# Kernel optimization log

Measured on AMD Instinct MI355X. Metric: run time of the kernel, lower is better.

## Reference

```python
import jax, jax.numpy as jnp
import numpy as np

B, HI, WI, DIM = 4, 128, 128, 128
HO, WO = HI // 2, WI // 2
NUM_ITERS = 3
EPS_LN, EPS_A = 1e-5, 1e-6


def _nbr_idx(H, W):
    # NATTEN kernel_size=3 neighborhood with border clamping: window center is
    # clip(i, 1, H-2) so every position sees exactly 9 neighbors.
    r = 1
    ci = jnp.clip(jnp.arange(H), r, H - 1 - r)
    cj = jnp.clip(jnp.arange(W), r, W - 1 - r)
    off = jnp.arange(-1, 2)
    ri = ci[:, None] + off[None, :]  # (H,3)
    rj = cj[:, None] + off[None, :]  # (W,3)
    nbr = jnp.broadcast_to(ri[:, None, :, None], (H, W, 3, 3)).reshape(H, W, 9)
    nbc = jnp.broadcast_to(rj[None, :, None, :], (H, W, 3, 3)).reshape(H, W, 9)
    return nbr, nbc


def _ln(x, g, b):
    mu = jnp.mean(x, -1, keepdims=True)
    var = jnp.mean(jnp.square(x - mu), -1, keepdims=True)
    return (x - mu) * jax.lax.rsqrt(var + EPS_LN) * g + b


def setup_inputs() -> dict:
    key = jax.random.key(0)
    ks = jax.random.split(key, 10)
    s = DIM ** -0.5
    return {
        "x": jax.random.normal(ks[0], (B, HI * WI, DIM), jnp.float32),
        "conv_w": jax.random.normal(ks[1], (DIM, DIM, 3, 3), jnp.float32) * (2.0 / (DIM * 9)) ** 0.5,
        "q_w": jax.random.normal(ks[2], (DIM, DIM), jnp.float32) * s,
        "k_w": jax.random.normal(ks[3], (DIM, DIM), jnp.float32) * s,
        "v_w": jax.random.normal(ks[4], (DIM, DIM), jnp.float32) * s,
        "mlp_w1": jax.random.normal(ks[5], (DIM, 2 * DIM), jnp.float32) * s,
        "mlp_b1": jnp.zeros((2 * DIM,), jnp.float32),
        "mlp_w2": jax.random.normal(ks[6], (2 * DIM, DIM), jnp.float32) * (2 * DIM) ** -0.5,
        "mlp_b2": jnp.zeros((DIM,), jnp.float32),
        "ln_in_g": jnp.ones((DIM,), jnp.float32),
        "ln_in_b": jnp.zeros((DIM,), jnp.float32),
        "ln_out_g": jnp.ones((DIM,), jnp.float32),
        "ln_out_b": jnp.zeros((DIM,), jnp.float32),
        "tau": jnp.asarray(np.log(DIM ** -0.5), jnp.float32),
        "rpb": jax.random.normal(ks[7], (4, 9), jnp.float32) * 0.02,
    }


def reference(x, conv_w, q_w, k_w, v_w, mlp_w1, mlp_b1, mlp_w2, mlp_b2,
              ln_in_g, ln_in_b, ln_out_g, ln_out_b, tau, rpb):
    Bx = x.shape[0]
    nbr, nbc = _nbr_idx(HO, WO)
    q_idx = (nbr * WO + nbc).reshape(HO * WO, 9)  # flat seed index of each neighbor

    def to_groups(t):  # (B, Hi*Wi, D) -> (B, 4, Ho, Wo, D); 4 = 2x2 patch pixels (row-major)
        m = t.transpose(0, 2, 1).reshape(Bx, DIM, HO, 2, WO, 2)
        return m.transpose(0, 3, 5, 2, 4, 1).reshape(Bx, 4, HO, WO, DIM)

    k = to_groups(_ln(x, ln_in_g, ln_in_b) @ k_w)
    v = to_groups(x @ v_w)
    v_nb = v[:, :, nbr, nbc, :]  # (B,4,Ho,Wo,9,D) value neighborhoods (loop-invariant)

    x_map = x.transpose(0, 2, 1).reshape(Bx, DIM, HI, WI)
    seed = jax.lax.conv_general_dilated(x_map, conv_w, (2, 2), ((1, 1), (1, 1)),
                                        dimension_numbers=('NCHW', 'OIHW', 'NCHW'))
    x_out = _ln(seed.reshape(Bx, DIM, HO * WO).transpose(0, 2, 1), ln_out_g, ln_out_b)

    scale = jnp.exp(tau)
    flat_idx = jnp.broadcast_to(q_idx[None], (4, HO * WO, 9)).reshape(-1)
    attn = A_col = None
    for _ in range(NUM_ITERS):
        q = _ln(x_out, ln_out_g, ln_out_b) @ q_w
        q_nb = q.reshape(Bx, HO, WO, DIM)[:, nbr, nbc, :]  # (B,Ho,Wo,9,D)
        # na2d_qk(query=k, key=q): logits at key-grid position vs seed neighbors
        attn = jnp.einsum('bghwd,bhwtd->bghwt', k, q_nb)
        attn = jax.nn.softmax((attn + rpb.reshape(1, 4, 1, 1, 9)) * scale, axis=-1) + EPS_A
        # scatter-based column sums over seed tokens (doubly-stochastic step)
        attn_flat = attn.reshape(Bx, -1)
        col_sums = jax.vmap(
            lambda a: jax.ops.segment_sum(a, flat_idx, num_segments=HO * WO))(attn_flat)
        denom = col_sums[:, q_idx]  # (B, Ho*Wo, 9) gather back per-edge
        A_col = (attn.reshape(Bx, 4, HO * WO, 9) / (denom[:, None] + 1e-8)).reshape(Bx, 4, HO, WO, 9)
        # na2d_av(A_col, v) then sum over the 4 patch-pixel groups
        upd = jnp.einsum('bghwt,bghwtd->bhwd', A_col, v_nb).reshape(Bx, HO * WO, DIM)
        x_out = x_out + upd
        h = jax.nn.gelu(x_out @ mlp_w1 + mlp_b1, approximate=False) @ mlp_w2 + mlp_b2
        x_out = x_out + _ln(h, ln_out_g, ln_out_b)
    return x_out, attn, A_col
```

## Files before the change

### kernel.cpp

```cpp
#include <hip/hip_runtime.h>
#include <hip/hip_bf16.h>
#include <math.h>

#define BN 4
#define HIq 128
#define WIq 128
#define DIM 128
#define HOq 64
#define WOq 64
#define NPOS 4096
#define NTOK 16384
#define EPS_LN 1e-5f
#define EPS_A 1e-6f

typedef __attribute__((ext_vector_type(8))) short bf16x8;
typedef __attribute__((ext_vector_type(4))) float f32x4;

__device__ __forceinline__ unsigned short f2bf(float f) {
    unsigned int u = __float_as_uint(f);
    u = (u + 0x7FFFu + ((u >> 16) & 1u)) >> 16;
    return (unsigned short)u;
}

__device__ __forceinline__ float bf2f(unsigned short u) {
    return __uint_as_float((unsigned int)u << 16);
}

__device__ __forceinline__ int nb_index(int h, int w, int t) {
    int ch = min(max(h, 1), HOq - 2);
    int cw = min(max(w, 1), WOq - 2);
    int dr = t / 3 - 1, dc = t % 3 - 1;
    return (ch + dr) * WOq + (cw + dc);
}

__global__ void prep_ln_kernel(const float* __restrict__ x,
                               const float* __restrict__ g,
                               const float* __restrict__ bb,
                               unsigned short* __restrict__ x_bf,
                               unsigned short* __restrict__ xln_bf) {
    int tid = threadIdx.x, wv = tid >> 6, lane = tid & 63;
    long row = (long)blockIdx.x * 4 + wv;
    const float2* xr = (const float2*)(x + row * DIM);
    float2 v = xr[lane];
    float s = v.x + v.y, ss = v.x * v.x + v.y * v.y;
    #pragma unroll
    for (int off = 32; off; off >>= 1) {
        s  += __shfl_xor(s, off, 64);
        ss += __shfl_xor(ss, off, 64);
    }
    float mu = s * (1.0f / DIM);
    float var = fmaxf(ss * (1.0f / DIM) - mu * mu, 0.0f);
    float rstd = rsqrtf(var + EPS_LN);
    float2 gg = ((const float2*)g)[lane];
    float2 bv = ((const float2*)bb)[lane];
    unsigned int xo = (unsigned int)f2bf(v.x) | ((unsigned int)f2bf(v.y) << 16);
    *(unsigned int*)&x_bf[row * DIM + 2 * lane] = xo;
    unsigned int lo = (unsigned int)f2bf((v.x - mu) * rstd * gg.x + bv.x)
                    | ((unsigned int)f2bf((v.y - mu) * rstd * gg.y + bv.y) << 16);
    *(unsigned int*)&xln_bf[row * DIM + 2 * lane] = lo;
}

__global__ void wt_prep_kernel(const float* __restrict__ cw,
                               const float* __restrict__ kw, const float* __restrict__ vw,
                               const float* __restrict__ qw,
                               const float* __restrict__ w1, const float* __restrict__ w2,
                               unsigned short* __restrict__ wt,
                               unsigned short* __restrict__ kwt, unsigned short* __restrict__ vwt,
                               unsigned short* __restrict__ qwt,
                               unsigned short* __restrict__ w1t, unsigned short* __restrict__ w2t) {
    int o = blockIdx.x, i = threadIdx.x;
    #pragma unroll
    for (int tap = 0; tap < 9; ++tap)
        wt[(long)o * 1152 + tap * 128 + i] = f2bf(cw[((long)o * 128 + i) * 9 + tap]);
    kwt[o * DIM + i] = f2bf(kw[i * DIM + o]);
    vwt[o * DIM + i] = f2bf(vw[i * DIM + o]);
    qwt[o * DIM + i] = f2bf(qw[i * DIM + o]);
    w1t[(2 * o) * DIM + i]     = f2bf(w1[i * 256 + 2 * o]);
    w1t[(2 * o + 1) * DIM + i] = f2bf(w1[i * 256 + 2 * o + 1]);
    w2t[o * 256 + i]       = f2bf(w2[i * DIM + o]);
    w2t[o * 256 + 128 + i] = f2bf(w2[(128 + i) * DIM + o]);
}

__global__ __launch_bounds__(256) void conv_mfma_kernel(
        const unsigned short* __restrict__ x_bf,
        const unsigned short* __restrict__ wt,
        const float* __restrict__ ln_g, const float* __restrict__ ln_b,
        float* __restrict__ out_x) {
    __shared__ __align__(16) char smem[52224];
    unsigned short (*As)[136] = (unsigned short(*)[136])smem;
    unsigned short (*Bs)[136] = (unsigned short(*)[136])(smem + 17408);
    float (*o_s)[132]         = (float(*)[132])smem;

    int tid = threadIdx.x;
    int wv = tid >> 6, lane = tid & 63;
    int quad = lane >> 4, l15 = lane & 15;
    int wr = wv >> 1, wc = wv & 1;
    int b = blockIdx.x >> 6, ho = blockIdx.x & 63;

    f32x4 acc[2][4];
    #pragma unroll
    for (int mt = 0; mt < 2; ++mt)
        #pragma unroll
        for (int nt = 0; nt < 4; ++nt) acc[mt][nt] = (f32x4){0.f, 0.f, 0.f, 0.f};

    for (int tap = 0; tap < 9; ++tap) {
        int kh = tap / 3, kw = tap % 3;
        int hi = 2 * ho - 1 + kh;
        bool hok = (hi >= 0) && (hi < HIq);
        __syncthreads();
        #pragma unroll
        for (int it = 0; it < 4; ++it) {
            int c = it * 256 + tid;
            int row = c >> 4, sg = c & 15;
            int wi = 2 * row - 1 + kw;
            int4 av = {0, 0, 0, 0};
            if (hok && wi >= 0 && wi < WIq)
                av = *(const int4*)(x_bf + (((long)b * HIq + hi) * WIq + wi) * DIM + sg * 8);
            *(int4*)&As[row][sg * 8] = av;
        }
        #pragma unroll
        for (int it = 0; it < 8; ++it) {
            int c = it * 256 + tid;
            int row = c >> 4, sg = c & 15;
            *(int4*)&Bs[row][sg * 8] =
                *(const int4*)(wt + (long)row * 1152 + tap * 128 + sg * 8);
        }
        __syncthreads();
        #pragma unroll
        for (int ib = 0; ib < 4; ++ib) {
            bf16x8 afr[2], bfr[4];
            #pragma unroll
            for (int mt = 0; mt < 2; ++mt)
                afr[mt] = *(bf16x8*)&As[wr * 32 + mt * 16 + l15][ib * 32 + quad * 8];
            #pragma unroll
            for (int nt = 0; nt < 4; ++nt)
                bfr[nt] = *(bf16x8*)&Bs[wc * 64 + nt * 16 + l15][ib * 32 + quad * 8];
            #pragma unroll
            for (int mt = 0; mt < 2; ++mt)
                #pragma unroll
                for (int nt = 0; nt < 4; ++nt)
                    acc[mt][nt] = __builtin_amdgcn_mfma_f32_16x16x32_bf16(
                        afr[mt], bfr[nt], acc[mt][nt], 0, 0, 0);
        }
    }
    __syncthreads();
    #pragma unroll
    for (int mt = 0; mt < 2; ++mt)
        #pragma unroll
        for (int r = 0; r < 4; ++r) {
            int wo = wr * 32 + mt * 16 + quad * 4 + r;
            #pragma unroll
            for (int nt = 0; nt < 4; ++nt) {
                int col = wc * 64 + nt * 16 + l15;
                o_s[wo][col] = acc[mt][nt][r];
            }
        }
    __syncthreads();

    {
        int r = tid >> 2, qq = tid & 3;
        float s = 0.f, ss = 0.f;
        #pragma unroll
        for (int j = 0; j < 32; ++j) {
            float v = o_s[r][qq * 32 + j];
            s += v; ss += v * v;
        }
        s  += __shfl_xor(s, 1, 64);  ss += __shfl_xor(ss, 1, 64);
        s  += __shfl_xor(s, 2, 64);  ss += __shfl_xor(ss, 2, 64);
        float mu = s * (1.0f / DIM);
        float var = fmaxf(ss * (1.0f / DIM) - mu * mu, 0.0f);
        float rstd = rsqrtf(var + EPS_LN);
        long outb = ((long)b * NPOS + ho * WOq) * DIM;
        float* xr = out_x + outb + (long)r * DIM + qq * 32;
        #pragma unroll
        for (int j = 0; j < 32; ++j) {
            int c = qq * 32 + j;
            xr[j] = (o_s[r][c] - mu) * rstd * ln_g[c] + ln_b[c];
        }
    }
}

__global__ __launch_bounds__(256) void kv_mfma_kernel(
        const unsigned short* __restrict__ x_bf,
        const unsigned short* __restrict__ xln_bf,
        const unsigned short* __restrict__ kwt,
        const unsigned short* __restrict__ vwt,
        unsigned short* __restrict__ k_bf, unsigned short* __restrict__ v_bf) {
    __shared__ unsigned short Ak[64][40], Av[64][40];
    __shared__ unsigned short Bk[128][40], Bv[128][40];
    int tid = threadIdx.x;
    int wv = tid >> 6, lane = tid & 63;
    int quad = lane >> 4, l15 = lane & 15;
    int wr = wv >> 1, wc = wv & 1;
    long tokBase = (long)blockIdx.x * 64;

    f32x4 acck[2][4], accv[2][4];
    #pragma unroll
    for (int mt = 0; mt < 2; ++mt)
        #pragma unroll
        for (int nt = 0; nt < 4; ++nt) {
            acck[mt][nt] = (f32x4){0.f, 0.f, 0.f, 0.f};
            accv[mt][nt] = (f32x4){0.f, 0.f, 0.f, 0.f};
        }

    int m = tid >> 2, seg = tid & 3;
    #pragma unroll
    for (int ib = 0; ib < 4; ++ib) {
        __syncthreads();
        *(int4*)&Ak[m][seg * 8] = *(const int4*)(xln_bf + (tokBase + m) * DIM + ib * 32 + seg * 8);
        *(int4*)&Av[m][seg * 8] = *(const int4*)(x_bf   + (tokBase + m) * DIM + ib * 32 + seg * 8);
        #pragma unroll
        for (int r2 = 0; r2 < 2; ++r2) {
            int lin = r2 * 256 + tid;
            int n = lin >> 2, sg = lin & 3;
            *(int4*)&Bk[n][sg * 8] = *(const int4*)(kwt + (long)n * DIM + ib * 32 + sg * 8);
            *(int4*)&Bv[n][sg * 8] = *(const int4*)(vwt + (long)n * DIM + ib * 32 + sg * 8);
        }
        __syncthreads();
        bf16x8 ak[2], av2[2], bk[4], bv[4];
        #pragma unroll
        for (int mt = 0; mt < 2; ++mt) {
            ak[mt]  = *(bf16x8*)&Ak[wr * 32 + mt * 16 + l15][quad * 8];
            av2[mt] = *(bf16x8*)&Av[wr * 32 + mt * 16 + l15][quad * 8];
        }
        #pragma unroll
        for (int nt = 0; nt < 4; ++nt) {
            bk[nt] = *(bf16x8*)&Bk[wc * 64 + nt * 16 + l15][quad * 8];
            bv[nt] = *(bf16x8*)&Bv[wc * 64 + nt * 16 + l15][quad * 8];
        }
        #pragma unroll
        for (int mt = 0; mt < 2; ++mt)
            #pragma unroll
            for (int nt = 0; nt < 4; ++nt) {
                acck[mt][nt] = __builtin_amdgcn_mfma_f32_16x16x32_bf16(ak[mt],  bk[nt], acck[mt][nt], 0, 0, 0);
                accv[mt][nt] = __builtin_amdgcn_mfma_f32_16x16x32_bf16(av2[mt], bv[nt], accv[mt][nt], 0, 0, 0);
            }
    }
    #pragma unroll
    for (int mt = 0; mt < 2; ++mt)
        #pragma unroll
        for (int r = 0; r < 4; ++r) {
            long tok = tokBase + wr * 32 + mt * 16 + quad * 4 + r;
            int b = (int)(tok >> 14);
            int pix = (int)(tok & 16383);
            int ih = pix >> 7, iw = pix & 127;
            int g = (ih & 1) * 2 + (iw & 1);
            int pos = (ih >> 1) * WOq + (iw >> 1);
            long base = ((long)(b * 4 + g) * NPOS + pos) * DIM;
            #pragma unroll
            for (int nt = 0; nt < 4; ++nt) {
                int col = wc * 64 + nt * 16 + l15;
                k_bf[base + col] = f2bf(acck[mt][nt][r]);
                v_bf[base + col] = f2bf(accv[mt][nt][r]);
            }
        }
}

__global__ __launch_bounds__(256) void q_mfma_kernel(
        const float* __restrict__ x_out,
        const unsigned short* __restrict__ qwt,
        const float* __restrict__ ln_g, const float* __restrict__ ln_b,
        unsigned short* __restrict__ q,
        float* __restrict__ col_sums) {
    __shared__ unsigned short sxbf[64][136];
    int tid = threadIdx.x;
    long base = (long)blockIdx.x * 64;

    int zi = blockIdx.x * 256 + tid;
    if (zi < BN * NPOS) col_sums[zi] = 0.0f;

    {
        int r = tid >> 2, qq = tid & 3;
        const float* xr = x_out + (base + r) * DIM + qq * 32;
        float vv[32];
        float s = 0.f, ss = 0.f;
        #pragma unroll
        for (int j = 0; j < 8; ++j) {
            float4 v4 = *(const float4*)(xr + j * 4);
            vv[j * 4 + 0] = v4.x; vv[j * 4 + 1] = v4.y;
            vv[j * 4 + 2] = v4.z; vv[j * 4 + 3] = v4.w;
            s += v4.x + v4.y + v4.z + v4.w;
            ss += v4.x * v4.x + v4.y * v4.y + v4.z * v4.z + v4.w * v4.w;
        }
        s  += __shfl_xor(s, 1, 64);  ss += __shfl_xor(ss, 1, 64);
        s  += __shfl_xor(s, 2, 64);  ss += __shfl_xor(ss, 2, 64);
        float mu = s * (1.0f / DIM);
        float var = fmaxf(ss * (1.0f / DIM) - mu * mu, 0.0f);
        float rstd = rsqrtf(var + EPS_LN);
        #pragma unroll
        for (int j = 0; j < 32; ++j) {
            int c = qq * 32 + j;
            sxbf[r][c] = f2bf((vv[j] - mu) * rstd * ln_g[c] + ln_b[c]);
        }
    }
    __syncthreads();

    int wv = tid >> 6, lane = tid & 63;
    int quad = lane >> 4, l15 = lane & 15;
    f32x4 acc[4][2];
    #pragma unroll
    for (int mt = 0; mt < 4; ++mt)
        #pragma unroll
        for (int nt = 0; nt < 2; ++nt) acc[mt][nt] = (f32x4){0.f, 0.f, 0.f, 0.f};

    #pragma unroll
    for (int kb = 0; kb < 4; ++kb) {
        bf16x8 afr[4], bfr[2];
        #pragma unroll
        for (int mt = 0; mt < 4; ++mt)
            afr[mt] = *(bf16x8*)&sxbf[mt * 16 + l15][kb * 32 + quad * 8];
        #pragma unroll
        for (int nt = 0; nt < 2; ++nt) {
            int n = wv * 32 + nt * 16 + l15;
            bfr[nt] = *(const bf16x8*)(qwt + (long)n * DIM + kb * 32 + quad * 8);
        }
        #pragma unroll
        for (int mt = 0; mt < 4; ++mt)
            #pragma unroll
            for (int nt = 0; nt < 2; ++nt)
                acc[mt][nt] = __builtin_amdgcn_mfma_f32_16x16x32_bf16(
                    afr[mt], bfr[nt], acc[mt][nt], 0, 0, 0);
    }
    #pragma unroll
    for (int mt = 0; mt < 4; ++mt)
        #pragma unroll
        for (int r = 0; r < 4; ++r) {
            long tok = base + mt * 16 + quad * 4 + r;
            #pragma unroll
            for (int nt = 0; nt < 2; ++nt) {
                int col = wv * 32 + nt * 16 + l15;
                q[tok * DIM + col] = f2bf(acc[mt][nt][r]);
            }
        }
}

__global__ __launch_bounds__(256) void attn_mfma_kernel(
        const unsigned short* __restrict__ k_bf,
        const unsigned short* __restrict__ q_bf,
        const float* __restrict__ rpb,
        const float* __restrict__ tau,
        float* __restrict__ attn_out,
        float* __restrict__ col_sums) {
    __shared__ __align__(16) char smem[69632];
    __shared__ float colacc[192];
    unsigned short (*Ks)[136] = (unsigned short(*)[136])smem;
    unsigned short (*Qs)[136] = (unsigned short(*)[136])(smem + 17408);
    float (*S)[193]           = (float(*)[193])smem;

    int tid = threadIdx.x;
    int bid = blockIdx.x;
    int h = bid & 63, g = (bid >> 6) & 3, b = bid >> 8;
    int r0 = min(max(h, 1), HOq - 2) - 1;

    long kbase = ((long)(b * 4 + g) * NPOS + h * 64) * DIM;
    long qbase = ((long)b * NPOS + r0 * 64) * DIM;

    if (tid < 192) colacc[tid] = 0.f;

    #pragma unroll
    for (int it = 0; it < 4; ++it) {
        int lin = it * 256 + tid;
        int row = lin >> 4, sg = lin & 15;
        *(int4*)&Ks[row][sg * 8] = *(const int4*)(k_bf + kbase + (long)row * DIM + sg * 8);
    }
    #pragma unroll
    for (int it = 0; it < 12; ++it) {
        int lin = it * 256 + tid;
        int row = lin >> 4, sg = lin & 15;
        *(int4*)&Qs[row][sg * 8] = *(const int4*)(q_bf + qbase + (long)row * DIM + sg * 8);
    }
    __syncthreads();

    int wv = tid >> 6, lane = tid & 63;
    int quad = lane >> 4, l15 = lane & 15;
    f32x4 acc[4][3];
    #pragma unroll
    for (int mt = 0; mt < 4; ++mt)
        #pragma unroll
        for (int nt = 0; nt < 3; ++nt) acc[mt][nt] = (f32x4){0.f, 0.f, 0.f, 0.f};

    #pragma unroll
    for (int kb = 0; kb < 4; ++kb) {
        bf16x8 afr[4], bfr[3];
        #pragma unroll
        for (int mt = 0; mt < 4; ++mt)
            afr[mt] = *(bf16x8*)&Ks[mt * 16 + l15][kb * 32 + quad * 8];
        #pragma unroll
        for (int nt = 0; nt < 3; ++nt)
            bfr[nt] = *(bf16x8*)&Qs[wv * 48 + nt * 16 + l15][kb * 32 + quad * 8];
        #pragma unroll
        for (int mt = 0; mt < 4; ++mt)
            #pragma unroll
            for (int nt = 0; nt < 3; ++nt)
                acc[mt][nt] = __builtin_amdgcn_mfma_f32_16x16x32_bf16(
                    afr[mt], bfr[nt], acc[mt][nt], 0, 0, 0);
    }
    __syncthreads();
    #pragma unroll
    for (int mt = 0; mt < 4; ++mt)
        #pragma unroll
        for (int nt = 0; nt < 3; ++nt)
            #pragma unroll
            for (int r = 0; r < 4; ++r)
                S[mt * 16 + quad * 4 + r][wv * 48 + nt * 16 + l15] = acc[mt][nt][r];
    __syncthreads();

    if (tid < 64) {
        int w = tid;
        int cw = min(max(w, 1), WOq - 2);
        float scale = expf(tau[0]);
        float l[9];
        #pragma unroll
        for (int t = 0; t < 9; ++t) {
            int j = (t / 3) * 64 + cw - 1 + (t % 3);
            l[t] = (S[w][j] + rpb[g * 9 + t]) * scale;
        }
        float m = l[0];
        #pragma unroll
        for (int t = 1; t < 9; ++t) m = fmaxf(m, l[t]);
        float e[9], s = 0.f;
        #pragma unroll
        for (int t = 0; t < 9; ++t) { e[t] = __expf(l[t] - m); s += e[t]; }
        float inv = 1.0f / s;
        long cell = (long)(b * 4 + g) * NPOS + h * 64 + w;
        #pragma unroll
        for (int t = 0; t < 9; ++t) {
            float a = e[t] * inv + EPS_A;
            int j = (t / 3) * 64 + cw - 1 + (t % 3);
            attn_out[cell * 9 + t] = a;
            atomicAdd(&colacc[j], a);
        }
    }
    __syncthreads();
    if (tid < 192) atomicAdd(&col_sums[b * NPOS + r0 * 64 + tid], colacc[tid]);
}

__global__ void acol_upd_kernel(const float* __restrict__ attn_out,
                                const float* __restrict__ col_sums,
                                const unsigned short* __restrict__ v_bf,
                                float* __restrict__ acol_out,
                                float* __restrict__ x_out) {
    __shared__ float sA[36];
    int tid = threadIdx.x;
    int row = blockIdx.x;
    int b = row >> 12, pos = row & 4095;
    int h = pos >> 6, w = pos & 63;

    if (tid < 36) {
        int g = tid / 9, t = tid % 9;
        long ci = ((long)(b * 4 + g) * NPOS + pos) * 9 + t;
        float a = attn_out[ci];
        float cs = col_sums[b * NPOS + nb_index(h, w, t)];
        float A = a / (cs + 1e-8f);
        sA[tid] = A;
        acol_out[ci] = A;
    }
    __syncthreads();

    int nn[9];
    #pragma unroll
    for (int t = 0; t < 9; ++t) nn[t] = nb_index(h, w, t);

    float acc = 0.f;
    #pragma unroll
    for (int g = 0; g < 4; ++g) {
        const unsigned short* vb = v_bf + (long)(b * 4 + g) * NPOS * DIM;
        #pragma unroll
        for (int t = 0; t < 9; ++t) {
            acc += sA[g * 9 + t] * bf2f(vb[(long)nn[t] * DIM + tid]);
        }
    }
    x_out[(long)row * DIM + tid] += acc;
}

__global__ __launch_bounds__(256) void mlp_mfma_kernel(
        float* __restrict__ x_out,
        const unsigned short* __restrict__ w1t,
        const unsigned short* __restrict__ w2t,
        const float* __restrict__ b1, const float* __restrict__ b2,
        const float* __restrict__ ln_g, const float* __restrict__ ln_b) {
    __shared__ __align__(16) char smem[25600];
    unsigned short (*sxbf)[136] = (unsigned short(*)[136])smem;
    unsigned short (*h_s)[264]  = (unsigned short(*)[264])(smem + 8704);
    float (*o_s)[132]           = (float(*)[132])smem;

    int tid = threadIdx.x;
    long base = (long)blockIdx.x * 32;
    int wv = tid >> 6, lane = tid & 63;
    int quad = lane >> 4, l15 = lane & 15;

    {
        int r = tid >> 3, seg = tid & 7;
        const float* xr = x_out + (base + r) * DIM + seg * 16;
        #pragma unroll
        for (int j = 0; j < 2; ++j) {
            float4 a = *(const float4*)(xr + j * 8);
            float4 c = *(const float4*)(xr + j * 8 + 4);
            unsigned short u[8] = {f2bf(a.x), f2bf(a.y), f2bf(a.z), f2bf(a.w),
                                   f2bf(c.x), f2bf(c.y), f2bf(c.z), f2bf(c.w)};
            *(int4*)&sxbf[r][seg * 16 + j * 8] = *(int4*)u;
        }
    }
    __syncthreads();

    f32x4 acc1[2][4];
    #pragma unroll
    for (int mt = 0; mt < 2; ++mt)
        #pragma unroll
        for (int nt = 0; nt < 4; ++nt) acc1[mt][nt] = (f32x4){0.f, 0.f, 0.f, 0.f};
    #pragma unroll
    for (int kb = 0; kb < 4; ++kb) {
        bf16x8 afr[2], bfr[4];
        #pragma unroll
        for (int mt = 0; mt < 2; ++mt)
            afr[mt] = *(bf16x8*)&sxbf[mt * 16 + l15][kb * 32 + quad * 8];
        #pragma unroll
        for (int nt = 0; nt < 4; ++nt) {
            int n = wv * 64 + nt * 16 + l15;
            bfr[nt] = *(const bf16x8*)(w1t + (long)n * DIM + kb * 32 + quad * 8);
        }
        #pragma unroll
        for (int mt = 0; mt < 2; ++mt)
            #pragma unroll
            for (int nt = 0; nt < 4; ++nt)
                acc1[mt][nt] = __builtin_amdgcn_mfma_f32_16x16x32_bf16(
                    afr[mt], bfr[nt], acc1[mt][nt], 0, 0, 0);
    }
    #pragma unroll
    for (int nt = 0; nt < 4; ++nt) {
        int col = wv * 64 + nt * 16 + l15;
        float bj = b1[col];
        #pragma unroll
        for (int mt = 0; mt < 2; ++mt)
            #pragma unroll
            for (int r = 0; r < 4; ++r) {
                int row = mt * 16 + quad * 4 + r;
                float hv = acc1[mt][nt][r] + bj;
                hv = 0.5f * hv * (1.0f + erff(hv * 0.70710678118654752f));
                h_s[row][col] = f2bf(hv);
            }
    }
    __syncthreads();

    f32x4 acc2[2][2];
    #pragma unroll
    for (int mt = 0; mt < 2; ++mt)
        #pragma unroll
        for (int nt = 0; nt < 2; ++nt) acc2[mt][nt] = (f32x4){0.f, 0.f, 0.f, 0.f};
    #pragma unroll
    for (int kb = 0; kb < 8; ++kb) {
        bf16x8 afr[2], bfr[2];
        #pragma unroll
        for (int mt = 0; mt < 2; ++mt)
            afr[mt] = *(bf16x8*)&h_s[mt * 16 + l15][kb * 32 + quad * 8];
        #pragma unroll
        for (int nt = 0; nt < 2; ++nt) {
            int n = wv * 32 + nt * 16 + l15;
            bfr[nt] = *(const bf16x8*)(w2t + (long)n * 256 + kb * 32 + quad * 8);
        }
        #pragma unroll
        for (int mt = 0; mt < 2; ++mt)
            #pragma unroll
            for (int nt = 0; nt < 2; ++nt)
                acc2[mt][nt] = __builtin_amdgcn_mfma_f32_16x16x32_bf16(
                    afr[mt], bfr[nt], acc2[mt][nt], 0, 0, 0);
    }
    __syncthreads();

    #pragma unroll
    for (int nt = 0; nt < 2; ++nt) {
        int col = wv * 32 + nt * 16 + l15;
        float bj = b2[col];
        #pragma unroll
        for (int mt = 0; mt < 2; ++mt)
            #pragma unroll
            for (int r = 0; r < 4; ++r)
                o_s[mt * 16 + quad * 4 + r][col] = acc2[mt][nt][r] + bj;
    }
    __syncthreads();

    {
        int r = tid >> 3, qq = tid & 7;
        float s = 0.f, ss = 0.f;
        #pragma unroll
        for (int j = 0; j < 16; ++j) {
            float v = o_s[r][qq * 16 + j];
            s += v; ss += v * v;
        }
        s  += __shfl_xor(s, 1, 64);  ss += __shfl_xor(ss, 1, 64);
        s  += __shfl_xor(s, 2, 64);  ss += __shfl_xor(ss, 2, 64);
        s  += __shfl_xor(s, 4, 64);  ss += __shfl_xor(ss, 4, 64);
        float mu = s * (1.0f / DIM);
        float var = fmaxf(ss * (1.0f / DIM) - mu * mu, 0.0f);
        float rstd = rsqrtf(var + EPS_LN);
        float* xr = x_out + (base + r) * DIM + qq * 16;
        #pragma unroll
        for (int j = 0; j < 16; ++j) {
            int c = qq * 16 + j;
            xr[j] = xr[j] + (o_s[r][c] - mu) * rstd * ln_g[c] + ln_b[c];
        }
    }
}

extern "C" void kernel_launch(void* const* d_in, const int* in_sizes, int n_in,
                              void* d_out, int out_size, void* d_ws, size_t ws_size,
                              hipStream_t stream) {
    const float* x        = (const float*)d_in[0];
    const float* conv_w   = (const float*)d_in[1];
    const float* q_w      = (const float*)d_in[2];
    const float* k_w      = (const float*)d_in[3];
    const float* v_w      = (const float*)d_in[4];
    const float* mlp_w1   = (const float*)d_in[5];
    const float* mlp_b1   = (const float*)d_in[6];
    const float* mlp_w2   = (const float*)d_in[7];
    const float* mlp_b2   = (const float*)d_in[8];
    const float* ln_in_g  = (const float*)d_in[9];
    const float* ln_in_b  = (const float*)d_in[10];
    const float* ln_out_g = (const float*)d_in[11];
    const float* ln_out_b = (const float*)d_in[12];
    const float* tau      = (const float*)d_in[13];
    const float* rpb      = (const float*)d_in[14];

    float* out_x    = (float*)d_out;
    float* out_attn = out_x + (long)BN * NPOS * DIM;
    float* out_acol = out_attn + (long)BN * 4 * NPOS * 9;

    char* ws = (char*)d_ws;
    unsigned short* k_bf = (unsigned short*)ws; ws += (long)BN * 4 * NPOS * DIM * 4;
    unsigned short* v_bf = (unsigned short*)ws; ws += (long)BN * 4 * NPOS * DIM * 4;
    unsigned short* x_bf = (unsigned short*)ws;
    unsigned short* q_bf = (unsigned short*)ws;
    ws += (long)BN * NTOK * DIM * 2;
    unsigned short* xln_bf = (unsigned short*)ws; ws += (long)BN * NTOK * DIM * 2;
    unsigned short* wt_conv = (unsigned short*)ws; ws += 1152L * DIM * 2;
    unsigned short* kwt = (unsigned short*)ws;     ws += (long)DIM * DIM * 2;
    unsigned short* vwt = (unsigned short*)ws;     ws += (long)DIM * DIM * 2;
    unsigned short* qwt = (unsigned short*)ws;     ws += (long)DIM * DIM * 2;
    unsigned short* w1t = (unsigned short*)ws;     ws += 256L * DIM * 2;
    unsigned short* w2t = (unsigned short*)ws;     ws += 256L * DIM * 2;
    float* col_sums = (float*)ws;       ws += (long)BN * NPOS * 4;

    prep_ln_kernel<<<16384, 256, 0, stream>>>(x, ln_in_g, ln_in_b, x_bf, xln_bf);
    wt_prep_kernel<<<128, 128, 0, stream>>>(conv_w, k_w, v_w, q_w, mlp_w1, mlp_w2,
                                            wt_conv, kwt, vwt, qwt, w1t, w2t);

    kv_mfma_kernel<<<1024, 256, 0, stream>>>(x_bf, xln_bf, kwt, vwt, k_bf, v_bf);
    conv_mfma_kernel<<<256, 256, 0, stream>>>(x_bf, wt_conv, ln_out_g, ln_out_b, out_x);

    for (int it = 0; it < 3; ++it) {
        q_mfma_kernel<<<256, 256, 0, stream>>>(out_x, qwt, ln_out_g, ln_out_b, q_bf, col_sums);
        attn_mfma_kernel<<<1024, 256, 0, stream>>>(k_bf, q_bf, rpb, tau, out_attn, col_sums);
        acol_upd_kernel<<<16384, 128, 0, stream>>>(out_attn, col_sums, v_bf, out_acol, out_x);
        mlp_mfma_kernel<<<512, 256, 0, stream>>>(out_x, w1t, w2t, mlp_b1, mlp_b2,
                                                 ln_out_g, ln_out_b);
    }
}
```

Before: 309.6 us.

## Tile acol_upd over 16-position row strips with shared-memory V halo reuse

The A_col/update kernel now gives each block a 16-position strip of one output row and stages the 3x18 neighborhood of V for each group into shared memory. It then computes the 9-tap weighted sums from LDS, replacing per-position redundant global gathers. The q projection kernel is also halved to 32 rows per block, doubling the grid to raise occupancy. The larger blocks add syncthreads per group and fewer, bigger blocks.

```diff
diff --git a/kernel.cpp b/kernel.cpp
--- a/kernel.cpp
+++ b/kernel.cpp
@@ -262,20 +262,20 @@
         const float* __restrict__ ln_g, const float* __restrict__ ln_b,
         unsigned short* __restrict__ q,
         float* __restrict__ col_sums) {
-    __shared__ unsigned short sxbf[64][136];
+    __shared__ unsigned short sxbf[32][136];
     int tid = threadIdx.x;
-    long base = (long)blockIdx.x * 64;
+    long base = (long)blockIdx.x * 32;
 
     int zi = blockIdx.x * 256 + tid;
     if (zi < BN * NPOS) col_sums[zi] = 0.0f;
 
     {
-        int r = tid >> 2, qq = tid & 3;
-        const float* xr = x_out + (base + r) * DIM + qq * 32;
-        float vv[32];
+        int r = tid >> 3, qq = tid & 7;
+        const float* xr = x_out + (base + r) * DIM + qq * 16;
+        float vv[16];
         float s = 0.f, ss = 0.f;
         #pragma unroll
-        for (int j = 0; j < 8; ++j) {
+        for (int j = 0; j < 4; ++j) {
             float4 v4 = *(const float4*)(xr + j * 4);
             vv[j * 4 + 0] = v4.x; vv[j * 4 + 1] = v4.y;
             vv[j * 4 + 2] = v4.z; vv[j * 4 + 3] = v4.w;
@@ -284,12 +284,13 @@
         }
         s  += __shfl_xor(s, 1, 64);  ss += __shfl_xor(ss, 1, 64);
         s  += __shfl_xor(s, 2, 64);  ss += __shfl_xor(ss, 2, 64);
+        s  += __shfl_xor(s, 4, 64);  ss += __shfl_xor(ss, 4, 64);
         float mu = s * (1.0f / DIM);
         float var = fmaxf(ss * (1.0f / DIM) - mu * mu, 0.0f);
         float rstd = rsqrtf(var + EPS_LN);
         #pragma unroll
-        for (int j = 0; j < 32; ++j) {
-            int c = qq * 32 + j;
+        for (int j = 0; j < 16; ++j) {
+            int c = qq * 16 + j;
             sxbf[r][c] = f2bf((vv[j] - mu) * rstd * ln_g[c] + ln_b[c]);
         }
     }
@@ -297,17 +298,17 @@
 
     int wv = tid >> 6, lane = tid & 63;
     int quad = lane >> 4, l15 = lane & 15;
-    f32x4 acc[4][2];
-    #pragma unroll
-    for (int mt = 0; mt < 4; ++mt)
+    f32x4 acc[2][2];
+    #pragma unroll
+    for (int mt = 0; mt < 2; ++mt)
         #pragma unroll
         for (int nt = 0; nt < 2; ++nt) acc[mt][nt] = (f32x4){0.f, 0.f, 0.f, 0.f};
 
     #pragma unroll
     for (int kb = 0; kb < 4; ++kb) {
-        bf16x8 afr[4], bfr[2];
-        #pragma unroll
-        for (int mt = 0; mt < 4; ++mt)
+        bf16x8 afr[2], bfr[2];
+        #pragma unroll
+        for (int mt = 0; mt < 2; ++mt)
             afr[mt] = *(bf16x8*)&sxbf[mt * 16 + l15][kb * 32 + quad * 8];
         #pragma unroll
         for (int nt = 0; nt < 2; ++nt) {
@@ -315,14 +316,14 @@
             bfr[nt] = *(const bf16x8*)(qwt + (long)n * DIM + kb * 32 + quad * 8);
         }
         #pragma unroll
-        for (int mt = 0; mt < 4; ++mt)
+        for (int mt = 0; mt < 2; ++mt)
             #pragma unroll
             for (int nt = 0; nt < 2; ++nt)
                 acc[mt][nt] = __builtin_amdgcn_mfma_f32_16x16x32_bf16(
                     afr[mt], bfr[nt], acc[mt][nt], 0, 0, 0);
     }
     #pragma unroll
-    for (int mt = 0; mt < 4; ++mt)
+    for (int mt = 0; mt < 2; ++mt)
         #pragma unroll
         for (int r = 0; r < 4; ++r) {
             long tok = base + mt * 16 + quad * 4 + r;
@@ -435,42 +436,66 @@
     if (tid < 192) atomicAdd(&col_sums[b * NPOS + r0 * 64 + tid], colacc[tid]);
 }
 
-__global__ void acol_upd_kernel(const float* __restrict__ attn_out,
-                                const float* __restrict__ col_sums,
-                                const unsigned short* __restrict__ v_bf,
-                                float* __restrict__ acol_out,
-                                float* __restrict__ x_out) {
-    __shared__ float sA[36];
+__global__ __launch_bounds__(256) void acol_upd_kernel(
+        const float* __restrict__ attn_out,
+        const float* __restrict__ col_sums,
+        const unsigned short* __restrict__ v_bf,
+        float* __restrict__ acol_out,
+        float* __restrict__ x_out) {
+    __shared__ unsigned short Vs[54 * 128];
+    __shared__ float sAg[16][9];
+    int bid = blockIdx.x;
+    int wt = bid & 3, h = (bid >> 2) & 63, b = bid >> 8;
+    int ch = min(max(h, 1), HOq - 2);
+    int r0 = ch - 1;
+    int c0 = min(max(16 * wt - 1, 0), 46);
     int tid = threadIdx.x;
-    int row = blockIdx.x;
-    int b = row >> 12, pos = row & 4095;
-    int h = pos >> 6, w = pos & 63;
-
-    if (tid < 36) {
-        int g = tid / 9, t = tid % 9;
-        long ci = ((long)(b * 4 + g) * NPOS + pos) * 9 + t;
-        float a = attn_out[ci];
-        float cs = col_sums[b * NPOS + nb_index(h, w, t)];
-        float A = a / (cs + 1e-8f);
-        sA[tid] = A;
-        acol_out[ci] = A;
-    }
-    __syncthreads();
-
-    int nn[9];
-    #pragma unroll
-    for (int t = 0; t < 9; ++t) nn[t] = nb_index(h, w, t);
-
-    float acc = 0.f;
-    #pragma unroll
+    int c = tid & 127, wg = tid >> 7;
+
+    float acc[8];
+    #pragma unroll
+    for (int k = 0; k < 8; ++k) acc[k] = 0.f;
+
     for (int g = 0; g < 4; ++g) {
-        const unsigned short* vb = v_bf + (long)(b * 4 + g) * NPOS * DIM;
-        #pragma unroll
-        for (int t = 0; t < 9; ++t) {
-            acc += sA[g * 9 + t] * bf2f(vb[(long)nn[t] * DIM + tid]);
-        }
-    }
-    x_out[(long)row * DIM + tid] += acc;
+        __syncthreads();
+        for (int idx = tid; idx < 864; idx += 256) {
+            int lr = idx >> 4, sg = idx & 15;
+            int rr = lr / 18, cc = lr % 18;
+            long goff = ((long)(b * 4 + g) * NPOS + (r0 + rr) * 64 + (c0 + cc)) * DIM;
+            *(int4*)&Vs[lr * 128 + sg * 8] = *(const int4*)(v_bf + goff + sg * 8);
+        }
+        if (tid < 144) {
+            int wl = tid / 9, t = tid % 9;
+            int w = wt * 16 + wl;
+            long ci = ((long)(b * 4 + g) * NPOS + h * 64 + w) * 9 + t;
+            float a = attn_out[ci];
+            float cs = col_sums[b * NPOS + nb_index(h, w, t)];
+            float A = a / (cs + 1e-8f);
+            sAg[wl][t] = A;
+            acol_out[ci] = A;
+        }
+        __syncthreads();
+        #pragma unroll
+        for (int k = 0; k < 8; ++k) {
+            int wl = wg * 8 + k;
+            int w = wt * 16 + wl;
+            int cw = min(max(w, 1), WOq - 2);
+            float a0 = 0.f;
+            #pragma unroll
+            for (int t = 0; t < 9; ++t) {
+                int rr = t / 3;
+                int cc = cw - 1 + (t % 3) - c0;
+                a0 += sAg[wl][t] * bf2f(Vs[(rr * 18 + cc) * 128 + c]);
+            }
+            acc[k] += a0;
+        }
+    }
+    long xbase = ((long)b * NPOS + h * 64 + wt * 16) * DIM;
+    #pragma unroll
+    for (int k = 0; k < 8; ++k) {
+        int wl = wg * 8 + k;
+        x_out[xbase + (long)wl * DIM + c] += acc[k];
+    }
 }
 
 __global__ __launch_bounds__(256) void mlp_mfma_kernel(
@@ -648,9 +673,9 @@
     conv_mfma_kernel<<<256, 256, 0, stream>>>(x_bf, wt_conv, ln_out_g, ln_out_b, out_x);
 
     for (int it = 0; it < 3; ++it) {
-        q_mfma_kernel<<<256, 256, 0, stream>>>(out_x, qwt, ln_out_g, ln_out_b, q_bf, col_sums);
+        q_mfma_kernel<<<512, 256, 0, stream>>>(out_x, qwt, ln_out_g, ln_out_b, q_bf, col_sums);
         attn_mfma_kernel<<<1024, 256, 0, stream>>>(k_bf, q_bf, rpb, tau, out_attn, col_sums);
-        acol_upd_kernel<<<16384, 128, 0, stream>>>(out_attn, col_sums, v_bf, out_acol, out_x);
+        acol_upd_kernel<<<1024, 256, 0, stream>>>(out_attn, col_sums, v_bf, out_acol, out_x);
         mlp_mfma_kernel<<<512, 256, 0, stream>>>(out_x, w1t, w2t, mlp_b1, mlp_b2,
                                                  ln_out_g, ln_out_b);
     }
```

Measured after the change: 324.3 us. +4.7%, slower.
